# Optimization experiments

Hardware: AMD Instinct MI355X
Metric: run time of the kernel (lower is better)

## Reference

```python
import jax, jax.numpy as jnp
import numpy as np

NUM_HEADS = 12   # H
NUM_TASKS = 4    # T
TOP_K = 2        # capacity_factor


def setup_inputs() -> dict:
    key = jax.random.key(0)
    ks = jax.random.split(key, 4)
    B, N, C = 2, 4100, 768  # N = NUM_TASKS + M, M = 4096
    x = jax.random.normal(ks[0], (B, N, C), dtype=jnp.float32)
    # torch.nn.Linear weights are [out_features, in_features]; y = x @ W.T
    qs_w = jax.random.normal(ks[1], (NUM_TASKS, C, C), dtype=jnp.float32) * 0.02
    kv_w = jax.random.normal(ks[2], (2 * C, C), dtype=jnp.float32) * 0.02
    experts_w = jax.random.normal(ks[3], (NUM_TASKS, C, C), dtype=jnp.float32) * 0.02
    return {"x": x, "qs_w": qs_w, "kv_w": kv_w, "experts_w": experts_w}


def reference(x, qs_w, kv_w, experts_w):
    B, N, C = x.shape
    T, H, K = NUM_TASKS, NUM_HEADS, TOP_K
    d = C // H
    M = N - T
    scale = d ** -0.5

    feature = x[:, T:, :]                                    # [B,M,C]
    kv = (feature @ kv_w.T).reshape(B, M, 2, H, d)
    k = jnp.transpose(kv[:, :, 0], (0, 2, 1, 3))             # [B,H,M,d]
    v = jnp.transpose(kv[:, :, 1], (0, 2, 1, 3))             # [B,H,M,d]

    # per-task q projections on task tokens (qs_w[t] is [out,in])
    q = jnp.einsum('btc,toc->bto', x[:, :T], qs_w)           # [B,T,C]
    q = q.reshape(B, T, H, d).transpose(0, 2, 1, 3)          # [B,H,T,d]

    attn = jnp.einsum('bhtd,bhmd->bhtm', q, k) * scale       # [B,H,T,M]
    topv, topi = jax.lax.top_k(attn, K)                      # [B,H,T,K]
    topw = jax.nn.softmax(topv, axis=-1)                     # softmax over top-k only

    # scatter softmaxed top-k back into dense [B,H,T,M] (indices unique per row)
    oh = jax.nn.one_hot(topi, M, dtype=x.dtype)              # [B,H,T,K,M]
    attn_topk = jnp.einsum('bhtk,bhtkm->bhtm', topw, oh)
    attn_token = jnp.einsum('bhtm,bhmd->bhtd', attn_topk, v)
    attn_token = attn_token.transpose(0, 2, 1, 3).reshape(B, T, C)   # [B,T,C]

    # gather top-k feature rows per head/task, weight, and scatter back
    fm = feature.reshape(B, M, H, d).transpose(0, 2, 1, 3)   # [B,H,M,d]
    feat_topk = jnp.take_along_axis(fm[:, :, None], topi[..., None], axis=3)  # [B,H,T,K,d]
    feat_topk = feat_topk * topw[..., None]
    # scatter to [B,H,T,M,d], then permute(0,2,3,1,4)+reshape -> [B,T,M,C]
    feat_pad = jnp.einsum('bhtkd,bhtkm->btmhd', feat_topk, oh).reshape(B, T, M, C)

    # per-task experts (no bias); einsum('btnc,btnc->bnc') with ones = sum over t
    feature_output = jnp.einsum('btmc,toc->bmo', feat_pad, experts_w)  # [B,M,C]
    token_output = jnp.einsum('btc,toc->bto', attn_token, experts_w)   # [B,T,C]

    return jnp.concatenate([token_output, feature_output], axis=1)     # [B,N,C]
```

## Files before the change

### kernel.cpp

```cpp
#include <hip/hip_runtime.h>
#include <math.h>

#define B_ 2
#define N_ 4100
#define C_ 768
#define T_ 4
#define H_ 12
#define D_ 64
#define M_ 4096
#define S_ 48
#define KS_ 6
#define KC_ 128
#define SEG_ 8
#define GRID_ 768
#define SCALE 0.125f

__device__ __forceinline__ bool better(float va, int ia, float vb, int ib) {
  return (va > vb) || (va == vb && ia < ib);
}

__device__ __forceinline__ void merge2(float& v1, int& i1, float& v2, int& i2,
                                       float ov1, int oi1, float ov2, int oi2) {
  if (better(ov1, oi1, v1, i1)) {
    float tv; int ti;
    tv = v1; ti = i1; v1 = ov1; i1 = oi1; ov1 = tv; oi1 = ti;
    tv = v2; ti = i2; v2 = ov2; i2 = oi2; ov2 = tv; oi2 = ti;
  }
  if (better(ov1, oi1, v2, i2)) { v2 = ov1; i2 = oi1; }
}

__global__ __launch_bounds__(256) void qkzero_kernel(const float* __restrict__ x,
    const float* __restrict__ qs_w, const float* __restrict__ kv_w,
    float* __restrict__ qk, float* __restrict__ out) {
  const int blk = blockIdx.x;
  const int tid = threadIdx.x;
  if (blk < B_ * S_) {
    const int h = blk % H_;
    const int t = (blk / H_) % T_;
    const int b = blk / S_;
    __shared__ float xs[C_];
    __shared__ float red[256];
    __shared__ float qseg[D_];
    for (int i = tid; i < C_; i += 256) xs[i] = x[((size_t)b * N_ + t) * C_ + i];
    __syncthreads();
    {
      const int j = tid & 63;
      const int pt = tid >> 6;
      const float* wr = qs_w + ((size_t)t * C_ + h * D_ + j) * C_ + pt * 192;
      float a = 0.f;
      for (int c = 0; c < 192; ++c) a += xs[pt * 192 + c] * wr[c];
      red[tid] = a;
    }
    __syncthreads();
    if (tid < 64)
      qseg[tid] = (red[tid] + red[tid + 64] + red[tid + 128] + red[tid + 192]) * SCALE;
    __syncthreads();
    for (int c = tid; c < C_; c += 256) {
      float a = 0.f;
      #pragma unroll 8
      for (int j = 0; j < 64; ++j) a += qseg[j] * kv_w[((size_t)(h * D_ + j)) * C_ + c];
      qk[(size_t)blk * C_ + c] = a;
    }
  } else {
    const int zb = blk - B_ * S_;
    const int NV4 = (B_ * N_ * C_) / 4;
    float4 z = make_float4(0.f, 0.f, 0.f, 0.f);
    float4* ov = (float4*)out;
    for (int i = zb * 256 + tid; i < NV4; i += (GRID_ - B_ * S_) * 256) ov[i] = z;
  }
}

__global__ __launch_bounds__(256) void score_kernel(const float* __restrict__ x,
    const float* __restrict__ qk, float* __restrict__ part) {
  const int mt = blockIdx.x & 63;
  const int b = blockIdx.x >> 6;
  const int kc = blockIdx.y;
  const int tid = threadIdx.x;
  const int m0 = mt * 64;

  __shared__ __align__(16) float fbuf[64][68];
  __shared__ __align__(16) float qkbuf[48][68];

  const int mg = tid & 15;
  const int sg = tid >> 4;

  float acc[4][3];
  #pragma unroll
  for (int u = 0; u < 4; ++u)
    #pragma unroll
    for (int i = 0; i < 3; ++i) acc[u][i] = 0.f;

  const float* xb = x + ((size_t)b * N_ + T_ + m0) * C_ + kc * KC_;
  const float* qkb = qk + (size_t)b * S_ * C_ + kc * KC_;

  for (int cc = 0; cc < KC_ / 64; ++cc) {
    __syncthreads();
    for (int i = tid; i < 64 * 16; i += 256) {
      int row = i >> 4, c4 = i & 15;
      *(float4*)&fbuf[row][c4 * 4] =
          *(const float4*)(xb + (size_t)row * C_ + cc * 64 + c4 * 4);
    }
    for (int i = tid; i < 48 * 16; i += 256) {
      int s = i >> 4, c4 = i & 15;
      *(float4*)&qkbuf[s][c4 * 4] =
          *(const float4*)(qkb + (size_t)s * C_ + cc * 64 + c4 * 4);
    }
    __syncthreads();
    #pragma unroll 4
    for (int c4 = 0; c4 < 16; ++c4) {
      float4 f[4], q[3];
      f[0] = *(const float4*)&fbuf[mg][c4 * 4];
      f[1] = *(const float4*)&fbuf[mg + 16][c4 * 4];
      f[2] = *(const float4*)&fbuf[mg + 32][c4 * 4];
      f[3] = *(const float4*)&fbuf[mg + 48][c4 * 4];
      q[0] = *(const float4*)&qkbuf[sg * 3 + 0][c4 * 4];
      q[1] = *(const float4*)&qkbuf[sg * 3 + 1][c4 * 4];
      q[2] = *(const float4*)&qkbuf[sg * 3 + 2][c4 * 4];
      #pragma unroll
      for (int u = 0; u < 4; ++u)
        #pragma unroll
        for (int i = 0; i < 3; ++i)
          acc[u][i] += f[u].x * q[i].x + f[u].y * q[i].y +
                       f[u].z * q[i].z + f[u].w * q[i].w;
    }
  }

  #pragma unroll
  for (int i = 0; i < 3; ++i) {
    int s = sg * 3 + i;
    float* pp = part + (((size_t)kc * B_ + b) * S_ + s) * M_ + m0 + mg;
    #pragma unroll
    for (int u = 0; u < 4; ++u) pp[16 * u] = acc[u][i];
  }
}

__global__ __launch_bounds__(256) void reduce_kernel(const float* __restrict__ part,
                                                     float* __restrict__ cand) {
  const int seg = blockIdx.x & 7;
  const int bs = blockIdx.x >> 3;
  const int tid = threadIdx.x;
  const size_t kstride = (size_t)B_ * S_ * M_;
  const float* p0 = part + (size_t)bs * M_ + seg * 512 + tid * 2;
  float a0 = 0.f, a1 = 0.f;
  #pragma unroll
  for (int kc = 0; kc < KS_; ++kc) {
    float2 v = *(const float2*)(p0 + kc * kstride);
    a0 += v.x; a1 += v.y;
  }
  const int mA = seg * 512 + tid * 2;
  float v1, v2; int i1, i2;
  if (better(a0, mA, a1, mA + 1)) { v1 = a0; i1 = mA; v2 = a1; i2 = mA + 1; }
  else                            { v1 = a1; i1 = mA + 1; v2 = a0; i2 = mA; }
  #pragma unroll
  for (int off = 1; off < 64; off <<= 1) {
    float ov1 = __shfl_xor(v1, off);
    int   oi1 = __shfl_xor(i1, off);
    float ov2 = __shfl_xor(v2, off);
    int   oi2 = __shfl_xor(i2, off);
    merge2(v1, i1, v2, i2, ov1, oi1, ov2, oi2);
  }
  __shared__ float cbuf[4][4];
  const int w = tid >> 6, lane = tid & 63;
  if (lane == 0) {
    cbuf[w][0] = v1; ((int*)cbuf[w])[1] = i1;
    cbuf[w][2] = v2; ((int*)cbuf[w])[3] = i2;
  }
  __syncthreads();
  if (tid == 0) {
    for (int ww = 1; ww < 4; ++ww)
      merge2(v1, i1, v2, i2, cbuf[ww][0], ((int*)cbuf[ww])[1],
             cbuf[ww][2], ((int*)cbuf[ww])[3]);
    ((float4*)cand)[blockIdx.x] =
        make_float4(v1, __int_as_float(i1), v2, __int_as_float(i2));
  }
}

__global__ __launch_bounds__(256) void gather_kernel(const float* __restrict__ x,
    const float* __restrict__ kv_w, const float* __restrict__ experts_w,
    const float* __restrict__ cand, float* __restrict__ out) {
  const int h = blockIdx.x % H_;
  const int t = (blockIdx.x / H_) % T_;
  const int b = blockIdx.x / S_;
  const int tid = threadIdx.x;

  __shared__ float f0[C_], f1[C_], fc[C_], red[256];
  __shared__ float attnh[D_];
  __shared__ float sel[4];

  if (tid < 8) {
    float4 cv = ((const float4*)cand)[blockIdx.x * 8 + tid];
    float v1 = cv.x, v2 = cv.z;
    int i1 = __float_as_int(cv.y), i2 = __float_as_int(cv.w);
    #pragma unroll
    for (int off = 1; off < 8; off <<= 1) {
      float ov1 = __shfl_xor(v1, off);
      int   oi1 = __shfl_xor(i1, off);
      float ov2 = __shfl_xor(v2, off);
      int   oi2 = __shfl_xor(i2, off);
      merge2(v1, i1, v2, i2, ov1, oi1, ov2, oi2);
    }
    if (tid == 0) {
      float w1 = 1.f / (1.f + expf(v2 - v1));
      ((int*)sel)[0] = i1; ((int*)sel)[1] = i2;
      sel[2] = w1; sel[3] = 1.f - w1;
    }
  }
  __syncthreads();
  const int i1 = ((const int*)sel)[0];
  const int i2 = ((const int*)sel)[1];
  const float w1 = sel[2], w2 = sel[3];

  const float* r0 = x + ((size_t)b * N_ + T_ + i1) * C_;
  const float* r1 = x + ((size_t)b * N_ + T_ + i2) * C_;
  for (int i = tid; i < C_; i += 256) {
    float a = r0[i], bb = r1[i];
    f0[i] = a; f1[i] = bb; fc[i] = w1 * a + w2 * bb;
  }
  __syncthreads();

  const int j = tid & 63, pt = tid >> 6;
  {
    const float* kr = kv_w + ((size_t)(C_ + h * D_ + j)) * C_ + pt * 192;
    float a = 0.f;
    for (int c = 0; c < 192; ++c) a += fc[pt * 192 + c] * kr[c];
    red[tid] = a;
  }
  __syncthreads();
  if (tid < 64)
    attnh[tid] = red[tid] + red[tid + 64] + red[tid + 128] + red[tid + 192];
  __syncthreads();

  const size_t ot = ((size_t)b * N_ + t) * C_;
  const size_t o0 = ((size_t)b * N_ + T_ + i1) * C_;
  const size_t o1 = ((size_t)b * N_ + T_ + i2) * C_;
  for (int o = tid; o < C_; o += 256) {
    const float* er = experts_w + ((size_t)t * C_ + o) * C_ + h * D_;
    float at = 0.f, a0 = 0.f, a1 = 0.f;
    #pragma unroll 8
    for (int c = 0; c < D_; ++c) {
      float e = er[c];
      at += e * attnh[c];
      a0 += e * f0[h * D_ + c];
      a1 += e * f1[h * D_ + c];
    }
    atomicAdd(&out[ot + o], at);
    atomicAdd(&out[o0 + o], w1 * a0);
    atomicAdd(&out[o1 + o], w2 * a1);
  }
}

extern "C" void kernel_launch(void* const* d_in, const int* in_sizes, int n_in,
                              void* d_out, int out_size, void* d_ws, size_t ws_size,
                              hipStream_t stream) {
  const float* x         = (const float*)d_in[0];
  const float* qs_w      = (const float*)d_in[1];
  const float* kv_w      = (const float*)d_in[2];
  const float* experts_w = (const float*)d_in[3];
  float* out = (float*)d_out;

  float* ws   = (float*)d_ws;
  float* qk   = ws;
  float* part = qk + (size_t)B_ * S_ * C_;
  float* cand = part + (size_t)KS_ * B_ * S_ * M_;

  hipLaunchKernelGGL(qkzero_kernel, dim3(GRID_),          dim3(256), 0, stream, x, qs_w, kv_w, qk, out);
  hipLaunchKernelGGL(score_kernel,  dim3(B_ * 64, KS_),   dim3(256), 0, stream, x, qk, part);
  hipLaunchKernelGGL(reduce_kernel, dim3(B_ * S_ * SEG_), dim3(256), 0, stream, part, cand);
  hipLaunchKernelGGL(gather_kernel, dim3(B_ * S_),        dim3(256), 0, stream, x, kv_w, experts_w, cand, out);
}
```

Before: 144.4 us.

## Fuse top-k reduction into gather kernel and double score kernel per-thread tile

```diff
diff --git a/kernel.cpp b/kernel.cpp
--- a/kernel.cpp
+++ b/kernel.cpp
@@ -11,7 +11,6 @@
 #define S_ 48
 #define KS_ 6
 #define KC_ 128
-#define SEG_ 8
 #define GRID_ 768
 #define SCALE 0.125f
 
@@ -70,7 +69,7 @@
   }
 }
 
-__global__ __launch_bounds__(256) void score_kernel(const float* __restrict__ x,
+__global__ __launch_bounds__(128) void score_kernel(const float* __restrict__ x,
     const float* __restrict__ qk, float* __restrict__ part) {
   const int mt = blockIdx.x & 63;
   const int b = blockIdx.x >> 6;
@@ -84,23 +83,23 @@
   const int mg = tid & 15;
   const int sg = tid >> 4;
 
-  float acc[4][3];
+  float acc[4][6];
   #pragma unroll
   for (int u = 0; u < 4; ++u)
     #pragma unroll
-    for (int i = 0; i < 3; ++i) acc[u][i] = 0.f;
+    for (int i = 0; i < 6; ++i) acc[u][i] = 0.f;
 
   const float* xb = x + ((size_t)b * N_ + T_ + m0) * C_ + kc * KC_;
   const float* qkb = qk + (size_t)b * S_ * C_ + kc * KC_;
 
   for (int cc = 0; cc < KC_ / 64; ++cc) {
     __syncthreads();
-    for (int i = tid; i < 64 * 16; i += 256) {
+    for (int i = tid; i < 64 * 16; i += 128) {
       int row = i >> 4, c4 = i & 15;
       *(float4*)&fbuf[row][c4 * 4] =
           *(const float4*)(xb + (size_t)row * C_ + cc * 64 + c4 * 4);
     }
-    for (int i = tid; i < 48 * 16; i += 256) {
+    for (int i = tid; i < 48 * 16; i += 128) {
       int s = i >> 4, c4 = i & 15;
       *(float4*)&qkbuf[s][c4 * 4] =
           *(const float4*)(qkb + (size_t)s * C_ + cc * 64 + c4 * 4);
@@ -108,104 +107,90 @@
     __syncthreads();
     #pragma unroll 4
     for (int c4 = 0; c4 < 16; ++c4) {
-      float4 f[4], q[3];
-      f[0] = *(const float4*)&fbuf[mg][c4 * 4];
-      f[1] = *(const float4*)&fbuf[mg + 16][c4 * 4];
-      f[2] = *(const float4*)&fbuf[mg + 32][c4 * 4];
-      f[3] = *(const float4*)&fbuf[mg + 48][c4 * 4];
-      q[0] = *(const float4*)&qkbuf[sg * 3 + 0][c4 * 4];
-      q[1] = *(const float4*)&qkbuf[sg * 3 + 1][c4 * 4];
-      q[2] = *(const float4*)&qkbuf[sg * 3 + 2][c4 * 4];
+      float4 f[4], q[6];
+      #pragma unroll
+      for (int u = 0; u < 4; ++u)
+        f[u] = *(const float4*)&fbuf[mg + 16 * u][c4 * 4];
+      #pragma unroll
+      for (int i = 0; i < 6; ++i)
+        q[i] = *(const float4*)&qkbuf[sg * 6 + i][c4 * 4];
       #pragma unroll
       for (int u = 0; u < 4; ++u)
         #pragma unroll
-        for (int i = 0; i < 3; ++i)
+        for (int i = 0; i < 6; ++i)
           acc[u][i] += f[u].x * q[i].x + f[u].y * q[i].y +
                        f[u].z * q[i].z + f[u].w * q[i].w;
     }
   }
 
   #pragma unroll
-  for (int i = 0; i < 3; ++i) {
-    int s = sg * 3 + i;
+  for (int i = 0; i < 6; ++i) {
+    int s = sg * 6 + i;
     float* pp = part + (((size_t)kc * B_ + b) * S_ + s) * M_ + m0 + mg;
     #pragma unroll
     for (int u = 0; u < 4; ++u) pp[16 * u] = acc[u][i];
-  }
-}
-
-__global__ __launch_bounds__(256) void reduce_kernel(const float* __restrict__ part,
-                                                     float* __restrict__ cand) {
-  const int seg = blockIdx.x & 7;
-  const int bs = blockIdx.x >> 3;
-  const int tid = threadIdx.x;
-  const size_t kstride = (size_t)B_ * S_ * M_;
-  const float* p0 = part + (size_t)bs * M_ + seg * 512 + tid * 2;
-  float a0 = 0.f, a1 = 0.f;
-  #pragma unroll
-  for (int kc = 0; kc < KS_; ++kc) {
-    float2 v = *(const float2*)(p0 + kc * kstride);
-    a0 += v.x; a1 += v.y;
-  }
-  const int mA = seg * 512 + tid * 2;
-  float v1, v2; int i1, i2;
-  if (better(a0, mA, a1, mA + 1)) { v1 = a0; i1 = mA; v2 = a1; i2 = mA + 1; }
-  else                            { v1 = a1; i1 = mA + 1; v2 = a0; i2 = mA; }
-  #pragma unroll
-  for (int off = 1; off < 64; off <<= 1) {
-    float ov1 = __shfl_xor(v1, off);
-    int   oi1 = __shfl_xor(i1, off);
-    float ov2 = __shfl_xor(v2, off);
-    int   oi2 = __shfl_xor(i2, off);
-    merge2(v1, i1, v2, i2, ov1, oi1, ov2, oi2);
-  }
-  __shared__ float cbuf[4][4];
-  const int w = tid >> 6, lane = tid & 63;
-  if (lane == 0) {
-    cbuf[w][0] = v1; ((int*)cbuf[w])[1] = i1;
-    cbuf[w][2] = v2; ((int*)cbuf[w])[3] = i2;
-  }
-  __syncthreads();
-  if (tid == 0) {
-    for (int ww = 1; ww < 4; ++ww)
-      merge2(v1, i1, v2, i2, cbuf[ww][0], ((int*)cbuf[ww])[1],
-             cbuf[ww][2], ((int*)cbuf[ww])[3]);
-    ((float4*)cand)[blockIdx.x] =
-        make_float4(v1, __int_as_float(i1), v2, __int_as_float(i2));
   }
 }
 
 __global__ __launch_bounds__(256) void gather_kernel(const float* __restrict__ x,
     const float* __restrict__ kv_w, const float* __restrict__ experts_w,
-    const float* __restrict__ cand, float* __restrict__ out) {
-  const int h = blockIdx.x % H_;
-  const int t = (blockIdx.x / H_) % T_;
-  const int b = blockIdx.x / S_;
+    const float* __restrict__ part, float* __restrict__ out) {
+  const int blk = blockIdx.x;
+  const int h = blk % H_;
+  const int t = (blk / H_) % T_;
+  const int b = blk / S_;
   const int tid = threadIdx.x;
 
   __shared__ float f0[C_], f1[C_], fc[C_], red[256];
   __shared__ float attnh[D_];
   __shared__ float sel[4];
-
-  if (tid < 8) {
-    float4 cv = ((const float4*)cand)[blockIdx.x * 8 + tid];
-    float v1 = cv.x, v2 = cv.z;
-    int i1 = __float_as_int(cv.y), i2 = __float_as_int(cv.w);
-    #pragma unroll
-    for (int off = 1; off < 8; off <<= 1) {
+  __shared__ float cbuf[4][4];
+
+  {
+    float v1 = -INFINITY, v2 = -INFINITY;
+    int i1 = 0x7fffffff, i2 = 0x7fffffff;
+    const float* p0 = part + (size_t)blk * M_;
+    const size_t kstride = (size_t)B_ * S_ * M_;
+    #pragma unroll
+    for (int ii = 0; ii < 4; ++ii) {
+      const int m = ii * 1024 + tid * 4;
+      float4 a = make_float4(0.f, 0.f, 0.f, 0.f);
+      #pragma unroll
+      for (int kc = 0; kc < KS_; ++kc) {
+        float4 v = *(const float4*)(p0 + kc * kstride + m);
+        a.x += v.x; a.y += v.y; a.z += v.z; a.w += v.w;
+      }
+      const float av[4] = {a.x, a.y, a.z, a.w};
+      #pragma unroll
+      for (int c = 0; c < 4; ++c) {
+        if (better(av[c], m + c, v1, i1)) { v2 = v1; i2 = i1; v1 = av[c]; i1 = m + c; }
+        else if (better(av[c], m + c, v2, i2)) { v2 = av[c]; i2 = m + c; }
+      }
+    }
+    #pragma unroll
+    for (int off = 1; off < 64; off <<= 1) {
       float ov1 = __shfl_xor(v1, off);
       int   oi1 = __shfl_xor(i1, off);
       float ov2 = __shfl_xor(v2, off);
       int   oi2 = __shfl_xor(i2, off);
       merge2(v1, i1, v2, i2, ov1, oi1, ov2, oi2);
     }
+    const int w = tid >> 6, lane = tid & 63;
+    if (lane == 0) {
+      cbuf[w][0] = v1; ((int*)cbuf[w])[1] = i1;
+      cbuf[w][2] = v2; ((int*)cbuf[w])[3] = i2;
+    }
+    __syncthreads();
     if (tid == 0) {
+      for (int ww = 1; ww < 4; ++ww)
+        merge2(v1, i1, v2, i2, cbuf[ww][0], ((int*)cbuf[ww])[1],
+               cbuf[ww][2], ((int*)cbuf[ww])[3]);
       float w1 = 1.f / (1.f + expf(v2 - v1));
       ((int*)sel)[0] = i1; ((int*)sel)[1] = i2;
       sel[2] = w1; sel[3] = 1.f - w1;
     }
-  }
-  __syncthreads();
+    __syncthreads();
+  }
   const int i1 = ((const int*)sel)[0];
   const int i2 = ((const int*)sel)[1];
   const float w1 = sel[2], w2 = sel[3];
@@ -261,10 +246,8 @@
   float* ws   = (float*)d_ws;
   float* qk   = ws;
   float* part = qk + (size_t)B_ * S_ * C_;
-  float* cand = part + (size_t)KS_ * B_ * S_ * M_;
-
-  hipLaunchKernelGGL(qkzero_kernel, dim3(GRID_),          dim3(256), 0, stream, x, qs_w, kv_w, qk, out);
-  hipLaunchKernelGGL(score_kernel,  dim3(B_ * 64, KS_),   dim3(256), 0, stream, x, qk, part);
-  hipLaunchKernelGGL(reduce_kernel, dim3(B_ * S_ * SEG_), dim3(256), 0, stream, part, cand);
-  hipLaunchKernelGGL(gather_kernel, dim3(B_ * S_),        dim3(256), 0, stream, x, kv_w, experts_w, cand, out);
-}
+
+  hipLaunchKernelGGL(qkzero_kernel, dim3(GRID_),        dim3(256), 0, stream, x, qs_w, kv_w, qk, out);
+  hipLaunchKernelGGL(score_kernel,  dim3(B_ * 64, KS_), dim3(128), 0, stream, x, qk, part);
+  hipLaunchKernelGGL(gather_kernel, dim3(B_ * S_),      dim3(256), 0, stream, x, kv_w, experts_w, part, out);
+}
```

Measured after the change: 151.5 us. 1.05x slower.
